# Kernel optimization log

Measured on AMD Instinct MI355X. Metric: run time of the kernel, lower is better.

Reference implementation:

```python
import jax, jax.numpy as jnp
import numpy as np

M_POW = 4   # m: number of visual-graph powers
N_POW = 4   # n: number of text-graph powers
T = 32      # temporal length, forced by torch.eye(32) in GraphFusion
EPS_BN = 1e-5


def conv1d_same(x, w, b):
    # x: (B, Cin, L), w: (Cout, Cin, 3) -> (B, Cout, L), padding=1
    y = jax.lax.conv_general_dilated(x, w, window_strides=(1,), padding=[(1, 1)],
                                     dimension_numbers=("NCH", "OIH", "NCH"))
    return y + b[None, :, None]


def setup_inputs() -> dict:
    key = jax.random.key(0)
    ks = jax.random.split(key, 10)
    b, c = 128, 5
    d = {}
    d["v_feature"] = jax.random.normal(ks[0], (b, c, T, 2048), jnp.float32)
    d["t_feature"] = jax.random.normal(ks[1], (b, c, T, 768), jnp.float32)
    # Temporal embedding convs (Conv1d k=3, pad=1)
    d["wv"] = jax.random.normal(ks[2], (32, 2048, 3), jnp.float32) * 0.02
    d["bv"] = jnp.zeros((32,), jnp.float32)
    d["wt"] = jax.random.normal(ks[3], (32, 768, 3), jnp.float32) * 0.02
    d["bt"] = jnp.zeros((32,), jnp.float32)
    # GraphFusion learned (m, n) bilinear matrix: torch.normal(0, 1)
    d["fusion_a"] = jax.random.normal(ks[4], (M_POW, N_POW), jnp.float32)
    # NormalHead (BN-WVAD style, in_channel=32, hidden 2 -> 1 -> 1, all k=1 convs)
    d["w1"] = jax.random.normal(ks[5], (2, 32), jnp.float32) * 0.1
    d["b1"] = jnp.zeros((2,), jnp.float32)
    d["g1"] = jnp.ones((2,), jnp.float32)
    d["be1"] = jnp.zeros((2,), jnp.float32)
    d["w2"] = jax.random.normal(ks[6], (1, 2), jnp.float32) * 0.1
    d["b2"] = jnp.zeros((1,), jnp.float32)
    d["g2"] = jnp.ones((1,), jnp.float32)
    d["be2"] = jnp.zeros((1,), jnp.float32)
    d["w3"] = jax.random.normal(ks[7], (1, 1), jnp.float32) * 0.1
    d["b3"] = jnp.zeros((1,), jnp.float32)
    return d


def _forward(v_feature, t_feature, wv, bv, wt, bt, fusion_a,
             w1, b1, g1, be1, w2, b2, g2, be2, w3, b3):
    b, c, t, feat_v = v_feature.shape
    B = b * c
    fv = v_feature.reshape(B, t, feat_v)
    ft = t_feature.reshape(B, t, t_feature.shape[3])
    # Temporal: permute -> conv1d(k=3,pad=1) -> relu -> permute
    fv = jax.nn.relu(conv1d_same(fv.transpose(0, 2, 1), wv, bv)).transpose(0, 2, 1)  # (B,t,32)
    ft = jax.nn.relu(conv1d_same(ft.transpose(0, 2, 1), wt, bt)).transpose(0, 2, 1)  # (B,t,32)

    # GraphFusion
    def l2n(x):
        return x / jnp.maximum(jnp.linalg.norm(x, axis=2, keepdims=True), 1e-12)
    f_v = l2n(fv)
    f_t = l2n(ft)
    a_v = jax.nn.relu(jnp.einsum('bid,bjd->bij', f_v, f_v))  # (B,t,t)
    a_t = jax.nn.relu(jnp.einsum('bid,bjd->bij', f_t, f_t))  # (B,t,t)
    eye = jnp.broadcast_to(jnp.eye(t, dtype=a_v.dtype), (B, t, t))
    # power 0 replaced by identity, as in the torch code
    av_p = jnp.stack([eye] + [a_v ** i for i in range(1, M_POW)], axis=0)  # (m,B,t,t)
    at_p = jnp.stack([eye] + [a_t ** j for j in range(1, N_POW)], axis=0)  # (n,B,t,t)
    # einsum('bijk,kl,blij->bij') with the permutes undone == 'kbij,kl,lbij->bij'
    a_fused = jnp.einsum('kbij,kl,lbij->bij', av_p, fusion_a, at_p)
    a_fused = jax.nn.relu(a_fused)
    a_fused = a_fused / (jnp.max(a_fused) + 0.01)

    # NormalHead on x = a_fused.permute(0,2,1) : (B, C=t, L=t)
    x = a_fused.transpose(0, 2, 1)

    def bn(h, g, beta):  # training-mode BatchNorm1d over (N, L) per channel
        mu = h.mean(axis=(0, 2), keepdims=True)
        var = h.var(axis=(0, 2), keepdims=True)
        return (h - mu) * jax.lax.rsqrt(var + EPS_BN) * g[None, :, None] + beta[None, :, None]

    x1 = jnp.einsum('oc,bcl->bol', w1, x) + b1[None, :, None]
    h1 = jax.nn.relu(bn(x1, g1, be1))
    x2 = jnp.einsum('oc,bcl->bol', w2, h1) + b2[None, :, None]
    h2 = jax.nn.relu(bn(x2, g2, be2))
    scores = jax.nn.sigmoid(jnp.einsum('oc,bcl->bol', w3, h2) + b3[None, :, None])  # (B,1,t)
    normal_scores = scores.reshape(b, c, t).mean(axis=1)  # (b, t), crop-averaged
    return (normal_scores, a_v, a_t, a_fused)


def reference(v_feature, t_feature, wv, bv, wt, bt, fusion_a,
              w1, b1, g1, be1, w2, b2, g2, be2, w3, b3):
    return _forward(v_feature, t_feature, wv, bv, wt, bt, fusion_a,
                    w1, b1, g1, be1, w2, b2, g2, be2, w3, b3)
```

## Files before the change

### kernel.cpp

```cpp
#include <hip/hip_runtime.h>
#include <math.h>


__global__ void pack_w_kernel(const float* __restrict__ src,
                              float* __restrict__ dst, int Cin) {
    int idx = blockIdx.x * 256 + threadIdx.x;
    int total = 32 * Cin * 3;
    if (idx >= total) return;
    int o = idx & 31;
    int k = (idx >> 5) % 3;
    int c = idx / 96;
    dst[idx] = src[(o * Cin + c) * 3 + k];
}

__global__ __launch_bounds__(256, 4) void conv_gemm_kernel(
    const float* __restrict__ x, const float* __restrict__ wP,
    const float* __restrict__ bias, float* __restrict__ y, int Cin) {
    int b = blockIdx.x;
    int tid = threadIdx.x;
    int wave = tid >> 6, lane = tid & 63;
    int t0 = (lane >> 3) * 4;
    int o0 = (lane & 7) * 4;
    __shared__ float smem[64 * 44 + 64 * 96];
    float* x_sh = smem;
    float* w_sh = smem + 64 * 44;
    float acc[4][4] = {{0.f}};
    const float* xb = x + (size_t)b * 32 * Cin;
    int nchunk = Cin >> 6;
    for (int ch = 0; ch < nchunk; ++ch) {
        __syncthreads();
        int c0 = ch << 6;
#pragma unroll
        for (int e = 0; e < 8; ++e) {
            int idx = tid + 256 * e;
            int t = idx >> 6, c = idx & 63;
            x_sh[c * 44 + t + 1] = xb[t * Cin + c0 + c];
        }
        if (tid < 64) { x_sh[tid * 44 + 0] = 0.f; x_sh[tid * 44 + 33] = 0.f; }
        const float4* wsrc = (const float4*)(wP + (size_t)c0 * 96);
        float4* wdst = (float4*)w_sh;
#pragma unroll
        for (int e = 0; e < 6; ++e) wdst[tid + 256 * e] = wsrc[tid + 256 * e];
        __syncthreads();
        const float* xr = x_sh + (wave * 16) * 44 + t0;
        const float* wr = w_sh + (wave * 16) * 96 + o0;
#pragma unroll 2
        for (int ci = 0; ci < 16; ++ci) {
            float4 xa = *(const float4*)(xr);
            float2 xc = *(const float2*)(xr + 4);
            float xv[6] = {xa.x, xa.y, xa.z, xa.w, xc.x, xc.y};
            float4 w0 = *(const float4*)(wr);
            float4 w1 = *(const float4*)(wr + 32);
            float4 w2 = *(const float4*)(wr + 64);
            float wk0[4] = {w0.x, w0.y, w0.z, w0.w};
            float wk1[4] = {w1.x, w1.y, w1.z, w1.w};
            float wk2[4] = {w2.x, w2.y, w2.z, w2.w};
#pragma unroll
            for (int i = 0; i < 4; ++i) {
#pragma unroll
                for (int j = 0; j < 4; ++j) {
                    float a = acc[i][j];
                    a = fmaf(xv[i],     wk0[j], a);
                    a = fmaf(xv[i + 1], wk1[j], a);
                    a = fmaf(xv[i + 2], wk2[j], a);
                    acc[i][j] = a;
                }
            }
            xr += 44; wr += 96;
        }
    }
    __syncthreads();
    float* red = smem;
#pragma unroll
    for (int i = 0; i < 4; ++i)
#pragma unroll
        for (int j = 0; j < 4; ++j)
            red[wave * 1024 + (t0 + i) * 32 + o0 + j] = acc[i][j];
    __syncthreads();
#pragma unroll
    for (int e = 0; e < 4; ++e) {
        int out = tid + 256 * e;
        float s = red[out] + red[1024 + out] + red[2048 + out] + red[3072 + out];
        y[(size_t)b * 1024 + out] = fmaxf(s + bias[out & 31], 0.f);
    }
}

__global__ __launch_bounds__(256) void s2_kernel(
    const float* __restrict__ fv, const float* __restrict__ ft,
    const float* __restrict__ fuse, float* __restrict__ out_av,
    float* __restrict__ out_at, float* __restrict__ out_af,
    unsigned int* __restrict__ maxslot) {
    int b = blockIdx.x, tid = threadIdx.x;
    __shared__ float Fv[32][33], Ft[32][33], inv[64], wmax[4];
#pragma unroll
    for (int e = 0; e < 4; ++e) {
        int idx = tid + 256 * e;
        int i = idx >> 5, j = idx & 31;
        Fv[i][j] = fv[b * 1024 + idx];
        Ft[i][j] = ft[b * 1024 + idx];
    }
    __syncthreads();
    if (tid < 64) {
        int i = tid & 31;
        float s = 0.f;
        if (tid < 32) {
            for (int c = 0; c < 32; ++c) { float v = Fv[i][c]; s = fmaf(v, v, s); }
        } else {
            for (int c = 0; c < 32; ++c) { float v = Ft[i][c]; s = fmaf(v, v, s); }
        }
        inv[tid] = 1.0f / fmaxf(sqrtf(s), 1e-12f);
    }
    __syncthreads();
    float fa[16];
#pragma unroll
    for (int q = 0; q < 16; ++q) fa[q] = fuse[q];
    float lmax = 0.f;
#pragma unroll
    for (int e = 0; e < 4; ++e) {
        int idx = tid + 256 * e;
        int i = idx >> 5, j = idx & 31;
        float dv = 0.f, dt_ = 0.f;
        for (int c = 0; c < 32; ++c) {
            dv  = fmaf(Fv[i][c], Fv[j][c], dv);
            dt_ = fmaf(Ft[i][c], Ft[j][c], dt_);
        }
        float av = fmaxf(dv  * inv[i] * inv[j], 0.f);
        float at = fmaxf(dt_ * inv[32 + i] * inv[32 + j], 0.f);
        out_av[b * 1024 + idx] = av;
        out_at[b * 1024 + idx] = at;
        float pv0 = (i == j) ? 1.f : 0.f;
        float pv1 = av, pv2 = av * av, pv3 = pv2 * av;
        float pt1 = at, pt2 = at * at, pt3 = pt2 * at;
        float af = 0.f;
        af += (fa[0] * pv0 + fa[4] * pv1 + fa[8]  * pv2 + fa[12] * pv3) * pv0;
        af += (fa[1] * pv0 + fa[5] * pv1 + fa[9]  * pv2 + fa[13] * pv3) * pt1;
        af += (fa[2] * pv0 + fa[6] * pv1 + fa[10] * pv2 + fa[14] * pv3) * pt2;
        af += (fa[3] * pv0 + fa[7] * pv1 + fa[11] * pv2 + fa[15] * pv3) * pt3;
        float r = fmaxf(af, 0.f);
        out_af[b * 1024 + idx] = r;
        lmax = fmaxf(lmax, r);
    }
    for (int off = 1; off < 64; off <<= 1)
        lmax = fmaxf(lmax, __shfl_xor(lmax, off));
    if ((tid & 63) == 0) wmax[tid >> 6] = lmax;
    __syncthreads();
    if (tid == 0) {
        float m = fmaxf(fmaxf(wmax[0], wmax[1]), fmaxf(wmax[2], wmax[3]));
        atomicMax(maxslot, __float_as_uint(m));
    }
}

__global__ __launch_bounds__(256) void s3_kernel(
    float* __restrict__ af, const float* __restrict__ w1,
    const float* __restrict__ b1, float* __restrict__ x1,
    float* __restrict__ scal) {
    int b = blockIdx.x, tid = threadIdx.x;
    __shared__ float A[32][33];
    float inv = 1.0f / (__uint_as_float(((const unsigned int*)scal)[0]) + 0.01f);
#pragma unroll
    for (int e = 0; e < 4; ++e) {
        int idx = tid + 256 * e;
        float v = af[b * 1024 + idx] * inv;
        af[b * 1024 + idx] = v;
        A[idx >> 5][idx & 31] = v;
    }
    __syncthreads();
    if (tid < 64) {
        int o = tid >> 5, l = tid & 31;
        float s = b1[o];
        for (int c = 0; c < 32; ++c) s = fmaf(w1[o * 32 + c], A[l][c], s);
        x1[(size_t)(b * 2 + o) * 32 + l] = s;
        float s1 = s, s2 = s * s;
        for (int off = 1; off < 32; off <<= 1) {
            s1 += __shfl_xor(s1, off);
            s2 += __shfl_xor(s2, off);
        }
        if (l == 0) {
            atomicAdd(&scal[1 + o], s1);
            atomicAdd(&scal[3 + o], s2);
        }
    }
}

__global__ __launch_bounds__(256) void s4_kernel(
    const float* __restrict__ x1, const float* __restrict__ g1,
    const float* __restrict__ be1, const float* __restrict__ w2,
    const float* __restrict__ b2, float* __restrict__ x2,
    float* __restrict__ scal) {
    int idx = blockIdx.x * 256 + threadIdx.x;
    const float N = 20480.f;
    float mu0 = scal[1] / N, mu1 = scal[2] / N;
    float va0 = scal[3] / N - mu0 * mu0, va1 = scal[4] / N - mu1 * mu1;
    float rs0 = rsqrtf(va0 + 1e-5f), rs1 = rsqrtf(va1 + 1e-5f);
    int b = idx >> 5, l = idx & 31;
    float h0 = fmaxf((x1[(size_t)(b * 2 + 0) * 32 + l] - mu0) * rs0 * g1[0] + be1[0], 0.f);
    float h1 = fmaxf((x1[(size_t)(b * 2 + 1) * 32 + l] - mu1) * rs1 * g1[1] + be1[1], 0.f);
    float v = w2[0] * h0 + w2[1] * h1 + b2[0];
    x2[idx] = v;
    float s1 = v, s2 = v * v;
    for (int off = 1; off < 64; off <<= 1) {
        s1 += __shfl_xor(s1, off);
        s2 += __shfl_xor(s2, off);
    }
    __shared__ float ps[4][2];
    int lane = threadIdx.x & 63, w = threadIdx.x >> 6;
    if (lane == 0) { ps[w][0] = s1; ps[w][1] = s2; }
    __syncthreads();
    if (threadIdx.x == 0) {
        atomicAdd(&scal[5], ps[0][0] + ps[1][0] + ps[2][0] + ps[3][0]);
        atomicAdd(&scal[6], ps[0][1] + ps[1][1] + ps[2][1] + ps[3][1]);
    }
}

__global__ __launch_bounds__(256) void s5_kernel(
    const float* __restrict__ x2, const float* __restrict__ g2,
    const float* __restrict__ be2, const float* __restrict__ w3,
    const float* __restrict__ b3, float* __restrict__ ns,
    const float* __restrict__ scal) {
    int idx = blockIdx.x * 256 + threadIdx.x;
    const float N = 20480.f;
    float mu = scal[5] / N;
    float var = scal[6] / N - mu * mu;
    float rs = rsqrtf(var + 1e-5f);
    int bb = idx >> 5, t = idx & 31;
    float s = 0.f;
#pragma unroll
    for (int crop = 0; crop < 5; ++crop) {
        int b = bb * 5 + crop;
        float h = fmaxf((x2[b * 32 + t] - mu) * rs * g2[0] + be2[0], 0.f);
        float z = w3[0] * h + b3[0];
        s += 1.f / (1.f + expf(-z));
    }
    ns[idx] = s * 0.2f;
}

extern "C" void kernel_launch(void* const* d_in, const int* in_sizes, int n_in,
                              void* d_out, int out_size, void* d_ws, size_t ws_size,
                              hipStream_t stream) {
    const float* v_feat = (const float*)d_in[0];
    const float* t_feat = (const float*)d_in[1];
    const float* wv  = (const float*)d_in[2];
    const float* bv  = (const float*)d_in[3];
    const float* wt  = (const float*)d_in[4];
    const float* bt  = (const float*)d_in[5];
    const float* fuse= (const float*)d_in[6];
    const float* w1  = (const float*)d_in[7];
    const float* b1  = (const float*)d_in[8];
    const float* g1  = (const float*)d_in[9];
    const float* be1 = (const float*)d_in[10];
    const float* w2  = (const float*)d_in[11];
    const float* b2  = (const float*)d_in[12];
    const float* g2  = (const float*)d_in[13];
    const float* be2 = (const float*)d_in[14];
    const float* w3  = (const float*)d_in[15];
    const float* b3  = (const float*)d_in[16];

    float* ws   = (float*)d_ws;
    float* scal = ws;
    float* wvP  = ws + 16;
    float* wtP  = wvP + 196608;
    float* fv   = wtP + 73728;
    float* ft   = fv + 655360;
    float* x1   = ft + 655360;
    float* x2   = x1 + 40960;

    float* out_ns = (float*)d_out;
    float* out_av = out_ns + 4096;
    float* out_at = out_av + 655360;
    float* out_af = out_at + 655360;

    hipMemsetAsync(scal, 0, 16 * sizeof(float), stream);
    pack_w_kernel<<<768, 256, 0, stream>>>(wv, wvP, 2048);
    pack_w_kernel<<<288, 256, 0, stream>>>(wt, wtP, 768);
    conv_gemm_kernel<<<640, 256, 0, stream>>>(v_feat, wvP, bv, fv, 2048);
    conv_gemm_kernel<<<640, 256, 0, stream>>>(t_feat, wtP, bt, ft, 768);
    s2_kernel<<<640, 256, 0, stream>>>(fv, ft, fuse, out_av, out_at, out_af,
                                       (unsigned int*)scal);
    s3_kernel<<<640, 256, 0, stream>>>(out_af, w1, b1, x1, scal);
    s4_kernel<<<80, 256, 0, stream>>>(x1, g1, be1, w2, b2, x2, scal);
    s5_kernel<<<16, 256, 0, stream>>>(x2, g2, be2, w3, b3, out_ns, scal);
}
```

Measured before the change: 456.3 us.

## Split conv over channel halves with atomic accumulation and fuse launches

The two conv launches are merged into one kernel that also splits each sample's input channels into two halves, giving 2560 blocks that accumulate partial sums with atomicAdd. Bias and ReLU move into s2, which also computes row norms with a parallel shuffle reduction. Weight packing and zeroing of the scalar slot and output buffers are combined into one kernel, with coalesced reads from the source weights. Channel chunks shrink to 32 and global loads use float4, so the smaller shared-memory footprint allows higher occupancy. The cost is extra atomic traffic and a zero-fill pass over the fv/ft buffers.

```diff
diff --git a/kernel.cpp b/kernel.cpp
--- a/kernel.cpp
+++ b/kernel.cpp
@@ -2,53 +2,70 @@
 #include <math.h>
 
 
-__global__ void pack_w_kernel(const float* __restrict__ src,
-                              float* __restrict__ dst, int Cin) {
-    int idx = blockIdx.x * 256 + threadIdx.x;
-    int total = 32 * Cin * 3;
-    if (idx >= total) return;
-    int o = idx & 31;
-    int k = (idx >> 5) % 3;
-    int c = idx / 96;
-    dst[idx] = src[(o * Cin + c) * 3 + k];
-}
-
-__global__ __launch_bounds__(256, 4) void conv_gemm_kernel(
-    const float* __restrict__ x, const float* __restrict__ wP,
-    const float* __restrict__ bias, float* __restrict__ y, int Cin) {
-    int b = blockIdx.x;
-    int tid = threadIdx.x;
-    int wave = tid >> 6, lane = tid & 63;
+__global__ __launch_bounds__(256) void pack_kernel(
+    const float* __restrict__ wv, const float* __restrict__ wt,
+    float* __restrict__ wvP, float* __restrict__ wtP,
+    float* __restrict__ scal, float* __restrict__ zbuf, int nz) {
+    int gid = blockIdx.x * 256 + threadIdx.x;
+    if (gid < 16) scal[gid] = 0.f;
+    for (int i = gid; i < nz; i += gridDim.x * 256) zbuf[i] = 0.f;
+    const int NV = 32 * 2048 * 3;
+    const int NT = 32 * 768 * 3;
+    if (gid < NV) {
+        int o = gid / 6144, rem = gid % 6144;
+        int c = rem / 3, k = rem % 3;
+        wvP[c * 96 + k * 32 + o] = wv[gid];
+    } else if (gid < NV + NT) {
+        int s = gid - NV;
+        int o = s / 2304, rem = s % 2304;
+        int c = rem / 3, k = rem % 3;
+        wtP[c * 96 + k * 32 + o] = wt[s];
+    }
+}
+
+__global__ __launch_bounds__(256, 8) void conv_kernel(
+    const float* __restrict__ xv, const float* __restrict__ wvP,
+    const float* __restrict__ xt, const float* __restrict__ wtP,
+    float* __restrict__ yv, float* __restrict__ yt) {
+    int bid = blockIdx.x;
+    const float* x; const float* wP; float* y; int Cin;
+    if (bid < 1280) { x = xv; wP = wvP; y = yv; Cin = 2048; }
+    else { bid -= 1280; x = xt; wP = wtP; y = yt; Cin = 768; }
+    int Ch = Cin >> 1;
+    int b = bid >> 1, half = bid & 1;
+    int c0g = half * Ch;
+    int nchunk = Ch >> 5;
+    int tid = threadIdx.x, wave = tid >> 6, lane = tid & 63;
     int t0 = (lane >> 3) * 4;
     int o0 = (lane & 7) * 4;
-    __shared__ float smem[64 * 44 + 64 * 96];
+    __shared__ float smem[32 * 36 + 32 * 96];
     float* x_sh = smem;
-    float* w_sh = smem + 64 * 44;
+    float* w_sh = smem + 32 * 36;
     float acc[4][4] = {{0.f}};
-    const float* xb = x + (size_t)b * 32 * Cin;
-    int nchunk = Cin >> 6;
+    const float* xb = x + (size_t)b * 32 * Cin + c0g;
+    const float* wb = wP + (size_t)c0g * 96;
+    int ts = tid >> 3, i4 = (tid & 7) * 4;
     for (int ch = 0; ch < nchunk; ++ch) {
+        int c0 = ch << 5;
         __syncthreads();
-        int c0 = ch << 6;
-#pragma unroll
-        for (int e = 0; e < 8; ++e) {
-            int idx = tid + 256 * e;
-            int t = idx >> 6, c = idx & 63;
-            x_sh[c * 44 + t + 1] = xb[t * Cin + c0 + c];
-        }
-        if (tid < 64) { x_sh[tid * 44 + 0] = 0.f; x_sh[tid * 44 + 33] = 0.f; }
-        const float4* wsrc = (const float4*)(wP + (size_t)c0 * 96);
+        float4 xq = *(const float4*)(xb + (size_t)ts * Cin + c0 + i4);
+        x_sh[(i4 + 0) * 36 + ts + 1] = xq.x;
+        x_sh[(i4 + 1) * 36 + ts + 1] = xq.y;
+        x_sh[(i4 + 2) * 36 + ts + 1] = xq.z;
+        x_sh[(i4 + 3) * 36 + ts + 1] = xq.w;
+        if (tid < 32) { x_sh[tid * 36] = 0.f; x_sh[tid * 36 + 33] = 0.f; }
+        const float4* wsrc = (const float4*)(wb + (size_t)c0 * 96);
         float4* wdst = (float4*)w_sh;
 #pragma unroll
-        for (int e = 0; e < 6; ++e) wdst[tid + 256 * e] = wsrc[tid + 256 * e];
+        for (int e = 0; e < 3; ++e) wdst[tid + 256 * e] = wsrc[tid + 256 * e];
         __syncthreads();
-        const float* xr = x_sh + (wave * 16) * 44 + t0;
-        const float* wr = w_sh + (wave * 16) * 96 + o0;
-#pragma unroll 2
-        for (int ci = 0; ci < 16; ++ci) {
+        const float* xr = x_sh + (wave * 8) * 36 + t0;
+        const float* wr = w_sh + (wave * 8) * 96 + o0;
+#pragma unroll
+        for (int ci = 0; ci < 8; ++ci) {
             float4 xa = *(const float4*)(xr);
             float2 xc = *(const float2*)(xr + 4);
-            float xv[6] = {xa.x, xa.y, xa.z, xa.w, xc.x, xc.y};
+            float xvv[6] = {xa.x, xa.y, xa.z, xa.w, xc.x, xc.y};
             float4 w0 = *(const float4*)(wr);
             float4 w1 = *(const float4*)(wr + 32);
             float4 w2 = *(const float4*)(wr + 64);
@@ -60,13 +77,13 @@
 #pragma unroll
                 for (int j = 0; j < 4; ++j) {
                     float a = acc[i][j];
-                    a = fmaf(xv[i],     wk0[j], a);
-                    a = fmaf(xv[i + 1], wk1[j], a);
-                    a = fmaf(xv[i + 2], wk2[j], a);
+                    a = fmaf(xvv[i],     wk0[j], a);
+                    a = fmaf(xvv[i + 1], wk1[j], a);
+                    a = fmaf(xvv[i + 2], wk2[j], a);
                     acc[i][j] = a;
                 }
             }
-            xr += 44; wr += 96;
+            xr += 36; wr += 96;
         }
     }
     __syncthreads();
@@ -81,12 +98,13 @@
     for (int e = 0; e < 4; ++e) {
         int out = tid + 256 * e;
         float s = red[out] + red[1024 + out] + red[2048 + out] + red[3072 + out];
-        y[(size_t)b * 1024 + out] = fmaxf(s + bias[out & 31], 0.f);
+        atomicAdd(&y[(size_t)b * 1024 + out], s);
     }
 }
 
 __global__ __launch_bounds__(256) void s2_kernel(
-    const float* __restrict__ fv, const float* __restrict__ ft,
+    const float* __restrict__ fvp, const float* __restrict__ ftp,
+    const float* __restrict__ bv, const float* __restrict__ bt,
     const float* __restrict__ fuse, float* __restrict__ out_av,
     float* __restrict__ out_at, float* __restrict__ out_af,
     unsigned int* __restrict__ maxslot) {
@@ -96,19 +114,24 @@
     for (int e = 0; e < 4; ++e) {
         int idx = tid + 256 * e;
         int i = idx >> 5, j = idx & 31;
-        Fv[i][j] = fv[b * 1024 + idx];
-        Ft[i][j] = ft[b * 1024 + idx];
-    }
-    __syncthreads();
-    if (tid < 64) {
-        int i = tid & 31;
-        float s = 0.f;
-        if (tid < 32) {
-            for (int c = 0; c < 32; ++c) { float v = Fv[i][c]; s = fmaf(v, v, s); }
-        } else {
-            for (int c = 0; c < 32; ++c) { float v = Ft[i][c]; s = fmaf(v, v, s); }
-        }
-        inv[tid] = 1.0f / fmaxf(sqrtf(s), 1e-12f);
+        Fv[i][j] = fmaxf(fvp[b * 1024 + idx] + bv[j], 0.f);
+        Ft[i][j] = fmaxf(ftp[b * 1024 + idx] + bt[j], 0.f);
+    }
+    __syncthreads();
+    {
+        int row = tid >> 3, cg = (tid & 7) * 4;
+        float sv = 0.f, st = 0.f;
+#pragma unroll
+        for (int q = 0; q < 4; ++q) {
+            float v = Fv[row][cg + q]; sv = fmaf(v, v, sv);
+            float u = Ft[row][cg + q]; st = fmaf(u, u, st);
+        }
+        sv += __shfl_xor(sv, 1); sv += __shfl_xor(sv, 2); sv += __shfl_xor(sv, 4);
+        st += __shfl_xor(st, 1); st += __shfl_xor(st, 2); st += __shfl_xor(st, 4);
+        if ((tid & 7) == 0) {
+            inv[row]      = rsqrtf(fmaxf(sv, 1e-24f));
+            inv[32 + row] = rsqrtf(fmaxf(st, 1e-24f));
+        }
     }
     __syncthreads();
     float fa[16];
@@ -269,13 +292,10 @@
     float* out_at = out_av + 655360;
     float* out_af = out_at + 655360;
 
-    hipMemsetAsync(scal, 0, 16 * sizeof(float), stream);
-    pack_w_kernel<<<768, 256, 0, stream>>>(wv, wvP, 2048);
-    pack_w_kernel<<<288, 256, 0, stream>>>(wt, wtP, 768);
-    conv_gemm_kernel<<<640, 256, 0, stream>>>(v_feat, wvP, bv, fv, 2048);
-    conv_gemm_kernel<<<640, 256, 0, stream>>>(t_feat, wtP, bt, ft, 768);
-    s2_kernel<<<640, 256, 0, stream>>>(fv, ft, fuse, out_av, out_at, out_af,
-                                       (unsigned int*)scal);
+    pack_kernel<<<1056, 256, 0, stream>>>(wv, wt, wvP, wtP, scal, fv, 2 * 655360);
+    conv_kernel<<<2560, 256, 0, stream>>>(v_feat, wvP, t_feat, wtP, fv, ft);
+    s2_kernel<<<640, 256, 0, stream>>>(fv, ft, bv, bt, fuse, out_av, out_at,
+                                       out_af, (unsigned int*)scal);
     s3_kernel<<<640, 256, 0, stream>>>(out_af, w1, b1, x1, scal);
     s4_kernel<<<80, 256, 0, stream>>>(x1, g1, be1, w2, b2, x2, scal);
     s5_kernel<<<16, 256, 0, stream>>>(x2, g2, be2, w3, b3, out_ns, scal);
```

After: 424.4 us. 7.0% less time.
